# Performance work log

Measured on AMD Instinct MI355X. Metric: run time of the kernel, lower is better.

The kernel has to match this reference:

```python
import jax, jax.numpy as jnp
import numpy as np

N = 65536   # collocation points
D = 2       # input dim
C = 16      # num subdomains / partitions (4x4 grid)
PH = 128    # PoU hidden dim
PNMID = 2   # PoU middle (residual) layers: depth=4 -> 2 middle
SW = 256    # subnet width
SNMID = 2   # subnet middle layers: eqx MLP depth=3 -> 2 width->width layers


def setup_inputs() -> dict:
    key = jax.random.key(0)
    ks = jax.random.split(key, 8)

    def w(k, shape, fan_in):
        return jax.random.normal(k, shape, jnp.float32) / jnp.sqrt(jnp.float32(fan_in))

    x = jax.random.uniform(ks[0], (N, D), jnp.float32)  # points in [0,1]^2
    # 4x4 grid of axis-aligned subdomains covering [0,1]^2
    g = np.linspace(0.0, 1.0, 5)
    lo = np.stack(np.meshgrid(g[:-1], g[:-1], indexing='ij'), -1).reshape(-1, 2)
    hi = np.stack(np.meshgrid(g[1:], g[1:], indexing='ij'), -1).reshape(-1, 2)
    centers = jnp.asarray((lo + hi) / 2.0, jnp.float32)  # [C, D]
    scales = jnp.asarray((hi - lo) / 2.0, jnp.float32)   # [C, D]

    return dict(
        x=x, centers=centers, scales=scales,
        pou_W0=w(ks[1], (D, PH), D), pou_b0=jnp.zeros((PH,), jnp.float32),
        pou_Wmid=w(ks[2], (PNMID, PH, PH), PH), pou_bmid=jnp.zeros((PNMID, PH), jnp.float32),
        pou_Wl=w(ks[3], (PH, C), PH), pou_bl=jnp.zeros((C,), jnp.float32),
        sub_W0=w(ks[4], (C, D, SW), D), sub_b0=jnp.zeros((C, SW), jnp.float32),
        sub_Wmid=w(ks[5], (C, SNMID, SW, SW), SW), sub_bmid=jnp.zeros((C, SNMID, SW), jnp.float32),
        sub_Wl=w(ks[6], (C, SW, 1), SW), sub_bl=jnp.zeros((C, 1), jnp.float32),
    )


def reference(x, centers, scales,
              pou_W0, pou_b0, pou_Wmid, pou_bmid, pou_Wl, pou_bl,
              sub_W0, sub_b0, sub_Wmid, sub_bmid, sub_Wl, sub_bl):
    # --- PoU gating net: residual ReLU MLP + softmax over partitions ---
    h = jax.nn.relu(x @ pou_W0 + pou_b0)                  # [N, PH]
    for l in range(pou_Wmid.shape[0]):
        h = h + jax.nn.relu(h @ pou_Wmid[l] + pou_bmid[l])
    wgt = jax.nn.softmax(h @ pou_Wl + pou_bl, axis=-1)    # [N, C] window weights

    # --- per-subdomain input normalization + batched subnet MLPs (tanh) ---
    xn = (x[None, :, :] - centers[:, None, :]) / scales[:, None, :]  # [C, N, D]
    g = jnp.tanh(jnp.einsum('cnd,cdw->cnw', xn, sub_W0) + sub_b0[:, None, :])  # [C, N, SW]
    for l in range(sub_Wmid.shape[1]):
        g = jnp.tanh(jnp.einsum('cnw,cwv->cnv', g, sub_Wmid[:, l]) + sub_bmid[:, l][:, None, :])
    u = (jnp.einsum('cnw,cwo->cno', g, sub_Wl) + sub_bl[:, None, :])[:, :, 0]  # [C, N]

    # --- windowed weighted sum:  acc_n = sum_c w[n,c] * u[c,n] ---
    acc = jnp.einsum('nc,cn->n', wgt, u)                  # [N]

    # --- ansatz: hard Dirichlet BC on the unit box: u = acc * prod_d x_d (1-x_d) ---
    return acc * jnp.prod(x * (1.0 - x), axis=-1)
```

## Files before the change

kernel.cpp:

```cpp
#include <hip/hip_runtime.h>

#define NPTS 65536
#define CC 16
#define PH 128
#define SW 256
#define MB 64
#define SP 264

typedef _Float16 half8 __attribute__((ext_vector_type(8)));
typedef _Float16 half4 __attribute__((ext_vector_type(4)));
typedef _Float16 half2 __attribute__((ext_vector_type(2)));
typedef float float4_ __attribute__((ext_vector_type(4)));
typedef float float2_ __attribute__((ext_vector_type(2)));

__device__ __forceinline__ float fast_tanh(float x) {
    float e = __builtin_amdgcn_exp2f(x * 2.8853900817779268f);
    float r = __builtin_amdgcn_rcpf(e + 1.0f);
    return fmaf(-2.0f, r, 1.0f);
}

__device__ __forceinline__ half4 pack4(float a, float b, float c, float d) {
    half2 lo = __builtin_bit_cast(half2, __builtin_amdgcn_cvt_pkrtz(a, b));
    half2 hi = __builtin_bit_cast(half2, __builtin_amdgcn_cvt_pkrtz(c, d));
    half4 h;
    h[0] = lo[0]; h[1] = lo[1]; h[2] = hi[0]; h[3] = hi[1];
    return h;
}

__global__ __launch_bounds__(256) void prep_wt(const float* __restrict__ Wmid,
                                               _Float16* __restrict__ Wt) {
    __shared__ float T[64][65];
    int b = blockIdx.x;
    int cl = b >> 4;
    int tile = b & 15;
    int w0 = (tile >> 2) * 64, v0 = (tile & 3) * 64;
    int t = threadIdx.x;
    int col = t & 63, row4 = t >> 6;
    const float* src = Wmid + ((size_t)cl << 16);
#pragma unroll
    for (int rr = 0; rr < 16; ++rr) {
        int wl = rr * 4 + row4;
        T[wl][col] = src[(size_t)(w0 + wl) * 256 + v0 + col];
    }
    __syncthreads();
    _Float16* dst = Wt + ((size_t)cl << 16);
#pragma unroll
    for (int rr = 0; rr < 16; ++rr) {
        int v = rr * 4 + row4;
        dst[(size_t)(v0 + v) * 256 + w0 + col] = (_Float16)T[col][v];
    }
}

__global__ __launch_bounds__(256) void pou_kernel(
    const float* __restrict__ x, const float* __restrict__ W0,
    const float* __restrict__ b0, const float* __restrict__ Wmid,
    const float* __restrict__ bmid, const float* __restrict__ Wl,
    const float* __restrict__ bl, float* __restrict__ wgtT) {
    __shared__ float hA[64][PH + 1];
    int t = threadIdx.x;
    int p = t & 63;
    int g4 = __builtin_amdgcn_readfirstlane(t >> 6);
    int jb = g4 * 32;
    int n0 = blockIdx.x * 64;
    float x0 = x[(size_t)(n0 + p) * 2];
    float x1 = x[(size_t)(n0 + p) * 2 + 1];

#pragma unroll
    for (int jj = 0; jj < 32; ++jj) {
        int j = jb + jj;
        float a = x0 * W0[j] + x1 * W0[PH + j] + b0[j];
        hA[p][j] = a > 0.f ? a : 0.f;
    }
    __syncthreads();

    for (int l = 0; l < 2; ++l) {
        float acc[32];
#pragma unroll
        for (int jj = 0; jj < 32; ++jj) acc[jj] = bmid[l * PH + jb + jj];
        for (int k = 0; k < PH; ++k) {
            float hv = hA[p][k];
#pragma unroll
            for (int jj = 0; jj < 32; ++jj)
                acc[jj] += hv * Wmid[(l * PH + k) * PH + jb + jj];
        }
        float resv[32];
#pragma unroll
        for (int jj = 0; jj < 32; ++jj) resv[jj] = hA[p][jb + jj];
        __syncthreads();
#pragma unroll
        for (int jj = 0; jj < 32; ++jj) {
            float r = acc[jj] > 0.f ? acc[jj] : 0.f;
            hA[p][jb + jj] = resv[jj] + r;
        }
        __syncthreads();
    }

    int c4 = g4 * 4;
    float lacc[4];
#pragma unroll
    for (int cc = 0; cc < 4; ++cc) lacc[cc] = bl[c4 + cc];
    for (int k = 0; k < PH; ++k) {
        float hv = hA[p][k];
#pragma unroll
        for (int cc = 0; cc < 4; ++cc) lacc[cc] += hv * Wl[k * CC + c4 + cc];
    }
    __syncthreads();
#pragma unroll
    for (int cc = 0; cc < 4; ++cc) hA[p][c4 + cc] = lacc[cc];
    __syncthreads();

    if (t < 64) {
        float lg[CC];
#pragma unroll
        for (int c = 0; c < CC; ++c) lg[c] = hA[t][c];
        float m = lg[0];
#pragma unroll
        for (int c = 1; c < CC; ++c) m = fmaxf(m, lg[c]);
        float s = 0.f;
#pragma unroll
        for (int c = 0; c < CC; ++c) {
            lg[c] = __builtin_amdgcn_exp2f((lg[c] - m) * 1.4426950408889634f);
            s += lg[c];
        }
        float inv = 1.0f / s;
#pragma unroll
        for (int c = 0; c < CC; ++c)
            wgtT[(size_t)c * NPTS + n0 + t] = lg[c] * inv;
    }
}

__global__ __launch_bounds__(256, 4) void subnet_kernel(
    const float* __restrict__ x, const float* __restrict__ centers,
    const float* __restrict__ scales, const float* __restrict__ W0,
    const float* __restrict__ b0, const _Float16* __restrict__ Wt,
    const float* __restrict__ bmid, const float* __restrict__ Wl,
    const float* __restrict__ bl, const float* __restrict__ wgtT,
    float* __restrict__ out) {
    __shared__ _Float16 g[MB * SP];
    __shared__ float part[4][MB];
    int t = threadIdx.x;
    int c = blockIdx.y;
    int n0 = blockIdx.x * MB;

    {
        float cx0 = centers[c * 2], cx1 = centers[c * 2 + 1];
        float is0 = 1.0f / scales[c * 2], is1 = 1.0f / scales[c * 2 + 1];
        int ln = t & 63;
        int pb = (t >> 6) * 16;
        const float* W0c = W0 + (size_t)c * 2 * SW;
        float4_ w0 = *(const float4_*)&W0c[ln * 4];
        float4_ w1 = *(const float4_*)&W0c[SW + ln * 4];
        float4_ bb = *(const float4_*)&b0[c * SW + ln * 4];
#pragma unroll 4
        for (int p = 0; p < 16; ++p) {
            float2_ xv = *(const float2_*)&x[(size_t)(n0 + pb + p) * 2];
            float xn0 = (xv[0] - cx0) * is0;
            float xn1 = (xv[1] - cx1) * is1;
            float tv[4];
#pragma unroll
            for (int j = 0; j < 4; ++j)
                tv[j] = fast_tanh(fmaf(xn0, w0[j], fmaf(xn1, w1[j], bb[j])));
            *(half4*)&g[(pb + p) * SP + ln * 4] = pack4(tv[0], tv[1], tv[2], tv[3]);
        }
    }
    __syncthreads();

    int lane = t & 63;
    int wave = t >> 6;
    int quad = lane >> 4;
    int l16 = lane & 15;
    int mb = wave * 64;

    {
        const _Float16* Wp = Wt + (((size_t)(c * 2 + 0)) << 16);
        const _Float16* Arow = Wp + (mb + l16) * SW + quad * 8;
        const float* bp = bmid + (c * 2 + 0) * SW + mb + quad * 4;
        float4_ acc[4][4];
#pragma unroll
        for (int mt = 0; mt < 4; ++mt) {
            float4_ bv = *(const float4_*)&bp[mt * 16];
#pragma unroll
            for (int nt = 0; nt < 4; ++nt) acc[mt][nt] = bv;
        }
#pragma unroll
        for (int kt = 0; kt < 8; ++kt) {
            half8 a[4], b[4];
#pragma unroll
            for (int mt = 0; mt < 4; ++mt)
                a[mt] = *(const half8*)&Arow[mt * 16 * SW + kt * 32];
#pragma unroll
            for (int nt = 0; nt < 4; ++nt)
                b[nt] = *(const half8*)&g[(nt * 16 + l16) * SP + kt * 32 + quad * 8];
#pragma unroll
            for (int mt = 0; mt < 4; ++mt)
#pragma unroll
                for (int nt = 0; nt < 4; ++nt)
                    acc[mt][nt] = __builtin_amdgcn_mfma_f32_16x16x32_f16(
                        a[mt], b[nt], acc[mt][nt], 0, 0, 0);
        }
        __syncthreads();
#pragma unroll
        for (int mt = 0; mt < 4; ++mt) {
#pragma unroll
            for (int nt = 0; nt < 4; ++nt) {
                float t0 = fast_tanh(acc[mt][nt][0]);
                float t1 = fast_tanh(acc[mt][nt][1]);
                float t2 = fast_tanh(acc[mt][nt][2]);
                float t3 = fast_tanh(acc[mt][nt][3]);
                *(half4*)&g[(nt * 16 + l16) * SP + mb + mt * 16 + quad * 4] =
                    pack4(t0, t1, t2, t3);
            }
        }
        __syncthreads();
    }

    {
        const _Float16* Wp = Wt + (((size_t)(c * 2 + 1)) << 16);
        const _Float16* Arow = Wp + (mb + l16) * SW + quad * 8;
        const float* bp = bmid + (c * 2 + 1) * SW + mb + quad * 4;
        float4_ acc[4][4];
#pragma unroll
        for (int mt = 0; mt < 4; ++mt) {
            float4_ bv = *(const float4_*)&bp[mt * 16];
#pragma unroll
            for (int nt = 0; nt < 4; ++nt) acc[mt][nt] = bv;
        }
#pragma unroll
        for (int kt = 0; kt < 8; ++kt) {
            half8 a[4], b[4];
#pragma unroll
            for (int mt = 0; mt < 4; ++mt)
                a[mt] = *(const half8*)&Arow[mt * 16 * SW + kt * 32];
#pragma unroll
            for (int nt = 0; nt < 4; ++nt)
                b[nt] = *(const half8*)&g[(nt * 16 + l16) * SP + kt * 32 + quad * 8];
#pragma unroll
            for (int mt = 0; mt < 4; ++mt)
#pragma unroll
                for (int nt = 0; nt < 4; ++nt)
                    acc[mt][nt] = __builtin_amdgcn_mfma_f32_16x16x32_f16(
                        a[mt], b[nt], acc[mt][nt], 0, 0, 0);
        }
        const float* wlp = Wl + c * SW + mb + quad * 4;
        float s[4] = {0.f, 0.f, 0.f, 0.f};
#pragma unroll
        for (int mt = 0; mt < 4; ++mt) {
            float4_ wv = *(const float4_*)&wlp[mt * 16];
#pragma unroll
            for (int nt = 0; nt < 4; ++nt) {
                float t0 = fast_tanh(acc[mt][nt][0]);
                float t1 = fast_tanh(acc[mt][nt][1]);
                float t2 = fast_tanh(acc[mt][nt][2]);
                float t3 = fast_tanh(acc[mt][nt][3]);
                s[nt] += fmaf(t0, wv[0],
                          fmaf(t1, wv[1], fmaf(t2, wv[2], t3 * wv[3])));
            }
        }
#pragma unroll
        for (int nt = 0; nt < 4; ++nt) {
            s[nt] += __shfl_xor(s[nt], 16);
            s[nt] += __shfl_xor(s[nt], 32);
        }
        if (quad == 0) {
#pragma unroll
            for (int nt = 0; nt < 4; ++nt) part[wave][nt * 16 + l16] = s[nt];
        }
    }
    __syncthreads();
    if (t < MB) {
        int n = n0 + t;
        float uv = part[0][t] + part[1][t] + part[2][t] + part[3][t] + bl[c];
        float w = wgtT[(size_t)c * NPTS + n];
        float2_ xv = *(const float2_*)&x[(size_t)n * 2];
        float ans = (xv[0] * (1.f - xv[0])) * (xv[1] * (1.f - xv[1]));
        atomicAdd(&out[n], uv * w * ans);
    }
}

extern "C" void kernel_launch(void* const* d_in, const int* in_sizes, int n_in,
                              void* d_out, int out_size, void* d_ws, size_t ws_size,
                              hipStream_t stream) {
    const float* x = (const float*)d_in[0];
    const float* centers = (const float*)d_in[1];
    const float* scales = (const float*)d_in[2];
    const float* pou_W0 = (const float*)d_in[3];
    const float* pou_b0 = (const float*)d_in[4];
    const float* pou_Wmid = (const float*)d_in[5];
    const float* pou_bmid = (const float*)d_in[6];
    const float* pou_Wl = (const float*)d_in[7];
    const float* pou_bl = (const float*)d_in[8];
    const float* sub_W0 = (const float*)d_in[9];
    const float* sub_b0 = (const float*)d_in[10];
    const float* sub_Wmid = (const float*)d_in[11];
    const float* sub_bmid = (const float*)d_in[12];
    const float* sub_Wl = (const float*)d_in[13];
    const float* sub_bl = (const float*)d_in[14];
    float* out = (float*)d_out;

    _Float16* wt = (_Float16*)d_ws;
    float* wgtT = (float*)((char*)d_ws + (4u << 20));

    hipMemsetAsync(out, 0, (size_t)out_size * sizeof(float), stream);
    prep_wt<<<dim3(512), dim3(256), 0, stream>>>(sub_Wmid, wt);
    pou_kernel<<<dim3(NPTS / 64), dim3(256), 0, stream>>>(
        x, pou_W0, pou_b0, pou_Wmid, pou_bmid, pou_Wl, pou_bl, wgtT);
    subnet_kernel<<<dim3(NPTS / MB, CC), dim3(256), 0, stream>>>(
        x, centers, scales, sub_W0, sub_b0, wt, sub_bmid, sub_Wl, sub_bl,
        wgtT, out);
}
```

Baseline: 640.1 us.

## Fold tanh exp2 scale into weights, compute tanh before barrier, raise MFMA priority

Pre-multiplies the subnet weights and biases by 2/ln2 (during the fp16 weight transpose and at load time), so each tanh skips one multiply. Moves the first middle layer's tanh ahead of the __syncthreads, so other waves' transcendental work can overlap the barrier wait. Wraps the MFMA loops in s_setprio and packs each fp16 store as one 64-bit word. Scaling the fp16 weights by about 2.9 changes rounding slightly but stays well within fp16 range.

Measured after the change: 660.4 us. +3.2%, slower.

```diff
diff --git a/kernel.cpp b/kernel.cpp
--- a/kernel.cpp
+++ b/kernel.cpp
@@ -6,25 +6,26 @@
 #define SW 256
 #define MB 64
 #define SP 264
+#define TS 2.8853900817779268f
 
 typedef _Float16 half8 __attribute__((ext_vector_type(8)));
 typedef _Float16 half4 __attribute__((ext_vector_type(4)));
 typedef _Float16 half2 __attribute__((ext_vector_type(2)));
 typedef float float4_ __attribute__((ext_vector_type(4)));
 typedef float float2_ __attribute__((ext_vector_type(2)));
-
-__device__ __forceinline__ float fast_tanh(float x) {
-    float e = __builtin_amdgcn_exp2f(x * 2.8853900817779268f);
+typedef unsigned int uint2_ __attribute__((ext_vector_type(2)));
+
+__device__ __forceinline__ float tanh_e(float y) {
+    float e = __builtin_amdgcn_exp2f(y);
     float r = __builtin_amdgcn_rcpf(e + 1.0f);
     return fmaf(-2.0f, r, 1.0f);
 }
 
-__device__ __forceinline__ half4 pack4(float a, float b, float c, float d) {
-    half2 lo = __builtin_bit_cast(half2, __builtin_amdgcn_cvt_pkrtz(a, b));
-    half2 hi = __builtin_bit_cast(half2, __builtin_amdgcn_cvt_pkrtz(c, d));
-    half4 h;
-    h[0] = lo[0]; h[1] = lo[1]; h[2] = hi[0]; h[3] = hi[1];
-    return h;
+__device__ __forceinline__ void store_pk4(_Float16* p, float a, float b, float c, float d) {
+    uint2_ u;
+    u.x = __builtin_bit_cast(unsigned int, __builtin_amdgcn_cvt_pkrtz(a, b));
+    u.y = __builtin_bit_cast(unsigned int, __builtin_amdgcn_cvt_pkrtz(c, d));
+    *(uint2_*)p = u;
 }
 
 __global__ __launch_bounds__(256) void prep_wt(const float* __restrict__ Wmid,
@@ -47,7 +48,7 @@
 #pragma unroll
     for (int rr = 0; rr < 16; ++rr) {
         int v = rr * 4 + row4;
-        dst[(size_t)(v0 + v) * 256 + w0 + col] = (_Float16)T[col][v];
+        dst[(size_t)(v0 + v) * 256 + w0 + col] = (_Float16)(T[col][v] * TS);
     }
 }
 
@@ -151,6 +152,7 @@
         float4_ w0 = *(const float4_*)&W0c[ln * 4];
         float4_ w1 = *(const float4_*)&W0c[SW + ln * 4];
         float4_ bb = *(const float4_*)&b0[c * SW + ln * 4];
+        w0 *= TS; w1 *= TS; bb *= TS;
 #pragma unroll 4
         for (int p = 0; p < 16; ++p) {
             float2_ xv = *(const float2_*)&x[(size_t)(n0 + pb + p) * 2];
@@ -159,8 +161,8 @@
             float tv[4];
 #pragma unroll
             for (int j = 0; j < 4; ++j)
-                tv[j] = fast_tanh(fmaf(xn0, w0[j], fmaf(xn1, w1[j], bb[j])));
-            *(half4*)&g[(pb + p) * SP + ln * 4] = pack4(tv[0], tv[1], tv[2], tv[3]);
+                tv[j] = tanh_e(fmaf(xn0, w0[j], fmaf(xn1, w1[j], bb[j])));
+            store_pk4(&g[(pb + p) * SP + ln * 4], tv[0], tv[1], tv[2], tv[3]);
         }
     }
     __syncthreads();
@@ -179,9 +181,11 @@
 #pragma unroll
         for (int mt = 0; mt < 4; ++mt) {
             float4_ bv = *(const float4_*)&bp[mt * 16];
+            bv *= TS;
 #pragma unroll
             for (int nt = 0; nt < 4; ++nt) acc[mt][nt] = bv;
         }
+        __builtin_amdgcn_s_setprio(1);
 #pragma unroll
         for (int kt = 0; kt < 8; ++kt) {
             half8 a[4], b[4];
@@ -198,17 +202,24 @@
                     acc[mt][nt] = __builtin_amdgcn_mfma_f32_16x16x32_f16(
                         a[mt], b[nt], acc[mt][nt], 0, 0, 0);
         }
+        __builtin_amdgcn_s_setprio(0);
+#pragma unroll
+        for (int mt = 0; mt < 4; ++mt)
+#pragma unroll
+            for (int nt = 0; nt < 4; ++nt) {
+                acc[mt][nt][0] = tanh_e(acc[mt][nt][0]);
+                acc[mt][nt][1] = tanh_e(acc[mt][nt][1]);
+                acc[mt][nt][2] = tanh_e(acc[mt][nt][2]);
+                acc[mt][nt][3] = tanh_e(acc[mt][nt][3]);
+            }
         __syncthreads();
 #pragma unroll
         for (int mt = 0; mt < 4; ++mt) {
 #pragma unroll
             for (int nt = 0; nt < 4; ++nt) {
-                float t0 = fast_tanh(acc[mt][nt][0]);
-                float t1 = fast_tanh(acc[mt][nt][1]);
-                float t2 = fast_tanh(acc[mt][nt][2]);
-                float t3 = fast_tanh(acc[mt][nt][3]);
-                *(half4*)&g[(nt * 16 + l16) * SP + mb + mt * 16 + quad * 4] =
-                    pack4(t0, t1, t2, t3);
+                store_pk4(&g[(nt * 16 + l16) * SP + mb + mt * 16 + quad * 4],
+                          acc[mt][nt][0], acc[mt][nt][1],
+                          acc[mt][nt][2], acc[mt][nt][3]);
             }
         }
         __syncthreads();
@@ -222,9 +233,11 @@
 #pragma unroll
         for (int mt = 0; mt < 4; ++mt) {
             float4_ bv = *(const float4_*)&bp[mt * 16];
+            bv *= TS;
 #pragma unroll
             for (int nt = 0; nt < 4; ++nt) acc[mt][nt] = bv;
         }
+        __builtin_amdgcn_s_setprio(1);
 #pragma unroll
         for (int kt = 0; kt < 8; ++kt) {
             half8 a[4], b[4];
@@ -241,6 +254,7 @@
                     acc[mt][nt] = __builtin_amdgcn_mfma_f32_16x16x32_f16(
                         a[mt], b[nt], acc[mt][nt], 0, 0, 0);
         }
+        __builtin_amdgcn_s_setprio(0);
         const float* wlp = Wl + c * SW + mb + quad * 4;
         float s[4] = {0.f, 0.f, 0.f, 0.f};
 #pragma unroll
@@ -248,10 +262,10 @@
             float4_ wv = *(const float4_*)&wlp[mt * 16];
 #pragma unroll
             for (int nt = 0; nt < 4; ++nt) {
-                float t0 = fast_tanh(acc[mt][nt][0]);
-                float t1 = fast_tanh(acc[mt][nt][1]);
-                float t2 = fast_tanh(acc[mt][nt][2]);
-                float t3 = fast_tanh(acc[mt][nt][3]);
+                float t0 = tanh_e(acc[mt][nt][0]);
+                float t1 = tanh_e(acc[mt][nt][1]);
+                float t2 = tanh_e(acc[mt][nt][2]);
+                float t3 = tanh_e(acc[mt][nt][3]);
                 s[nt] += fmaf(t0, wv[0],
                           fmaf(t1, wv[1], fmaf(t2, wv[2], t3 * wv[3])));
             }
```
